# Performance work log

Hardware: AMD Instinct MI355X
Metric: run time of the kernel (lower is better)

Reference implementation:

```python
import jax, jax.numpy as jnp
import numpy as np

N_NODES = 100000
N_EDGES = 600000
N_GRAPHS = 64
EPS = 1e-5


def setup_inputs() -> dict:
    key = jax.random.key(0)
    ks = jax.random.split(key, 8)
    x = jax.random.normal(ks[0], (N_NODES, 128), dtype=jnp.float32)
    edge_index = jax.random.randint(ks[1], (2, N_EDGES), 0, N_NODES, dtype=jnp.int64)
    batch = jnp.sort(jax.random.randint(ks[2], (N_NODES,), 0, N_GRAPHS, dtype=jnp.int64))
    conv_w = jax.random.normal(ks[3], (6, 128, 128), dtype=jnp.float32) * (1.0 / np.sqrt(128))
    conv_b = jnp.zeros((6, 128), dtype=jnp.float32)
    bn_g = jnp.ones((6, 128), dtype=jnp.float32)
    bn_b = jnp.zeros((6, 128), dtype=jnp.float32)
    lin1_w = jax.random.normal(ks[4], (128, 64), dtype=jnp.float32) * (1.0 / np.sqrt(128))
    lin1_b = jnp.zeros((64,), dtype=jnp.float32)
    lin2_w = jax.random.normal(ks[5], (64, 4), dtype=jnp.float32) * (1.0 / np.sqrt(64))
    lin2_b = jnp.zeros((4,), dtype=jnp.float32)
    return {"x": x, "edge_index": edge_index, "batch": batch,
            "conv_w": conv_w, "conv_b": conv_b, "bn_g": bn_g, "bn_b": bn_b,
            "lin1_w": lin1_w, "lin1_b": lin1_b, "lin2_w": lin2_w, "lin2_b": lin2_b}


def reference(x, edge_index, batch, conv_w, conv_b, bn_g, bn_b, lin1_w, lin1_b, lin2_w, lin2_b):
    src, dst = edge_index[0], edge_index[1]  # messages flow src -> dst (PyG source_to_target)
    n = x.shape[0]
    h = x
    # 6 stacked GCNConv(normalize=False) -> ReLU -> BatchNorm1d (training-mode batch stats)
    for i in range(6):
        m = h @ conv_w[i]                                   # [N, H] transform first
        agg = jax.ops.segment_sum(m[src], dst, num_segments=n) + conv_b[i]
        h = jax.nn.relu(agg)
        mean = h.mean(axis=0)
        var = h.var(axis=0)                                  # biased, matches torch BN
        h = (h - mean) * jax.lax.rsqrt(var + EPS) * bn_g[i] + bn_b[i]
    # global mean pool over graphs
    s = jax.ops.segment_sum(h, batch, num_segments=N_GRAPHS)          # [G, H]
    cnt = jax.ops.segment_sum(jnp.ones((n,), h.dtype), batch, num_segments=N_GRAPHS)
    pooled = s / jnp.maximum(cnt, 1.0)[:, None]
    out = pooled @ lin1_w + lin1_b
    out = out @ lin2_w + lin2_b
    return jax.nn.log_softmax(out, axis=-1)
```

## Files before the change

kernel.cpp:

```cpp
#include <hip/hip_runtime.h>
#include <math.h>

#define NN 100000
#define NE 600000
#define NG 64
#define HD 128
#define NL 6
#define NB 1563
#define PSL 16

typedef unsigned short ushort_t;
typedef short short8 __attribute__((ext_vector_type(8)));
typedef float floatx4 __attribute__((ext_vector_type(4)));

__device__ __forceinline__ float bf2f(ushort_t u) {
    return __uint_as_float(((unsigned)u) << 16);
}
__device__ __forceinline__ ushort_t f2bf(float f) {
    unsigned u = __float_as_uint(f);
    unsigned r = (u + 0x7fffu + ((u >> 16) & 1u)) >> 16;
    return (ushort_t)r;
}


__global__ __launch_bounds__(256) void k_cast(const float* __restrict__ x,
                                              ushort_t* __restrict__ xb) {
    int i = blockIdx.x * 256 + threadIdx.x;
    if (i < NN * 32) {
        float4 v = ((const float4*)x)[i];
        ((ushort4*)xb)[i] = make_ushort4(f2bf(v.x), f2bf(v.y), f2bf(v.z), f2bf(v.w));
    }
}


__global__ __launch_bounds__(256) void k_wcast(const float* __restrict__ W,
                                               ushort_t* __restrict__ Wt) {
    const float* Wl = W + blockIdx.x * 16384;
    ushort_t* Wtl = Wt + blockIdx.x * 16384;
    for (int id = threadIdx.x; id < 16384; id += 256) {
        int k = id >> 7, c = id & 127;
        Wtl[c * 128 + k] = f2bf(Wl[id]);
    }
}


__global__ __launch_bounds__(256) void k_hist(const int* __restrict__ ei, int* __restrict__ counts) {
    int e = blockIdx.x * 256 + threadIdx.x;
    if (e < NE) atomicAdd(&counts[ei[NE + e]], 1);
}

__global__ __launch_bounds__(256) void k_scan1(const int* __restrict__ counts, int* __restrict__ bsums) {
    __shared__ int s[256];
    int i = blockIdx.x * 256 + threadIdx.x;
    s[threadIdx.x] = (i < NN) ? counts[i] : 0;
    __syncthreads();
    for (int off = 128; off > 0; off >>= 1) {
        if (threadIdx.x < off) s[threadIdx.x] += s[threadIdx.x + off];
        __syncthreads();
    }
    if (threadIdx.x == 0) bsums[blockIdx.x] = s[0];
}

__global__ __launch_bounds__(512) void k_scan2(int* __restrict__ bsums, int nb) {
    __shared__ int s[512];
    int t = threadIdx.x;
    s[t] = (t < nb) ? bsums[t] : 0;
    __syncthreads();
    for (int off = 1; off < 512; off <<= 1) {
        int v = (t >= off) ? s[t - off] : 0;
        __syncthreads();
        s[t] += v;
        __syncthreads();
    }
    if (t < nb) bsums[t] = (t == 0) ? 0 : s[t - 1];
}

__global__ __launch_bounds__(256) void k_scan3(const int* __restrict__ counts, const int* __restrict__ bsums,
                                               int* __restrict__ rowptr) {
    __shared__ int s[256];
    int t = threadIdx.x;
    int i = blockIdx.x * 256 + t;
    int v = (i < NN) ? counts[i] : 0;
    s[t] = v;
    __syncthreads();
    for (int off = 1; off < 256; off <<= 1) {
        int u = (t >= off) ? s[t - off] : 0;
        __syncthreads();
        s[t] += u;
        __syncthreads();
    }
    if (i < NN) rowptr[i] = bsums[blockIdx.x] + s[t] - v;
    if (i == 0) rowptr[NN] = NE;
}

__global__ __launch_bounds__(256) void k_fill(const int* __restrict__ ei, const int* __restrict__ rowptr,
                                              int* __restrict__ cursor, int* __restrict__ colsrc) {
    int e = blockIdx.x * 256 + threadIdx.x;
    if (e < NE) {
        int d = ei[NE + e];
        int pos = rowptr[d] + atomicAdd(&cursor[d], 1);
        colsrc[pos] = ei[e];
    }
}


__global__ __launch_bounds__(256) void k_dhist(const int* __restrict__ rowptr,
                                               int* __restrict__ dcount) {
    __shared__ int lc[64];
    int t = threadIdx.x;
    if (t < 64) lc[t] = 0;
    __syncthreads();
    int n = blockIdx.x * 256 + t;
    if (n < NN) {
        int d = rowptr[n + 1] - rowptr[n];
        atomicAdd(&lc[min(d, 63)], 1);
    }
    __syncthreads();
    if (t < 64 && lc[t] > 0) atomicAdd(&dcount[t], lc[t]);
}

__global__ __launch_bounds__(64) void k_dscan(const int* __restrict__ dcount,
                                              int* __restrict__ doff) {
    int t = threadIdx.x;
    int s = 0;
    for (int b = t + 1; b < 64; ++b) s += dcount[b];
    doff[t] = s;
}

__global__ __launch_bounds__(256) void k_dfill(const int* __restrict__ rowptr,
                                               const int* __restrict__ doff,
                                               int* __restrict__ dcursor,
                                               int* __restrict__ perm) {
    __shared__ int lc[64], lbase[64];
    int t = threadIdx.x;
    if (t < 64) lc[t] = 0;
    __syncthreads();
    int n = blockIdx.x * 256 + t;
    int b = 0, my = 0;
    if (n < NN) {
        int d = rowptr[n + 1] - rowptr[n];
        b = min(d, 63);
        my = atomicAdd(&lc[b], 1);
    }
    __syncthreads();
    if (t < 64 && lc[t] > 0) lbase[t] = atomicAdd(&dcursor[t], lc[t]);
    __syncthreads();
    if (n < NN) perm[doff[b] + lbase[b] + my] = n;
}


__global__ __launch_bounds__(256) void k_gconv(
    const ushort_t* __restrict__ hin, const int* __restrict__ perm,
    const int* __restrict__ rowptr, const int* __restrict__ colsrc,
    const float* __restrict__ stats, const float* __restrict__ bng,
    const float* __restrict__ bnb,
    const ushort_t* __restrict__ Wt, const float* __restrict__ bias,
    ushort_t* __restrict__ hout, float* __restrict__ partials) {
    __shared__ float sstat[256];
    int t = threadIdx.x;
    sstat[t] = 0.f;
    int wave = t >> 6, lane = t & 63;
    int l15 = lane & 15, quad = lane >> 4;
    int rowbase = blockIdx.x * 64 + wave * 16;
    int idx = rowbase + l15;
    bool valid = idx < NN;
    int row = valid ? perm[idx] : 0;
    int beg = valid ? rowptr[row] : 0;
    int end = valid ? rowptr[row + 1] : 0;
    int deg = end - beg;
    int maxd = deg;
    maxd = max(maxd, __shfl_xor(maxd, 1, 64));
    maxd = max(maxd, __shfl_xor(maxd, 2, 64));
    maxd = max(maxd, __shfl_xor(maxd, 4, 64));
    maxd = max(maxd, __shfl_xor(maxd, 8, 64));

    float ac[4][8];
    #pragma unroll
    for (int s = 0; s < 4; ++s)
        #pragma unroll
        for (int j = 0; j < 8; ++j) ac[s][j] = 0.f;

    const ushort_t* hbase = hin + quad * 8;
    int e = 0;
    for (; e + 1 < maxd; e += 2) {
        bool on0 = e < deg, on1 = e + 1 < deg;
        int i0 = on0 ? beg + e : 0;
        int i1 = on1 ? beg + e + 1 : 0;
        int s0 = colsrc[i0];
        int s1 = colsrc[i1];
        float m0 = on0 ? 1.f : 0.f;
        float m1 = on1 ? 1.f : 0.f;
        const short8* h0 = (const short8*)(hbase + (size_t)s0 * 128);
        const short8* h1 = (const short8*)(hbase + (size_t)s1 * 128);
        short8 v0[4], v1[4];
        #pragma unroll
        for (int s = 0; s < 4; ++s) { v0[s] = h0[s * 4]; v1[s] = h1[s * 4]; }
        #pragma unroll
        for (int s = 0; s < 4; ++s)
            #pragma unroll
            for (int j = 0; j < 8; ++j) {
                ac[s][j] = fmaf(m0, bf2f((ushort_t)v0[s][j]), ac[s][j]);
                ac[s][j] = fmaf(m1, bf2f((ushort_t)v1[s][j]), ac[s][j]);
            }
    }
    if (e < maxd) {
        bool on0 = e < deg;
        int i0 = on0 ? beg + e : 0;
        int s0 = colsrc[i0];
        float m0 = on0 ? 1.f : 0.f;
        const short8* h0 = (const short8*)(hbase + (size_t)s0 * 128);
        #pragma unroll
        for (int s = 0; s < 4; ++s) {
            short8 v0 = h0[s * 4];
            #pragma unroll
            for (int j = 0; j < 8; ++j)
                ac[s][j] = fmaf(m0, bf2f((ushort_t)v0[j]), ac[s][j]);
        }
    }

    float degf = (float)deg;
    short8 afrag[4];
    #pragma unroll
    for (int s = 0; s < 4; ++s) {
        short8 av;
        #pragma unroll
        for (int j = 0; j < 8; ++j) {
            int f = s * 32 + quad * 8 + j;
            float val;
            if (stats != nullptr) {
                const float inv_n = 1.0f / (float)NN;
                float m = stats[f] * inv_n;
                float var = fmaf(-m, m, stats[HD + f] * inv_n);
                float sc = bng[f] * rsqrtf(var + 1e-5f);
                float sh = bnb[f] - m * sc;
                val = fmaf(sc, ac[s][j], degf * sh);
            } else {
                val = ac[s][j];
            }
            av[j] = (short)f2bf(val);
        }
        afrag[s] = av;
    }

    floatx4 acc[8];
    #pragma unroll
    for (int c = 0; c < 8; ++c) acc[c] = (floatx4){0.f, 0.f, 0.f, 0.f};
    #pragma unroll
    for (int c = 0; c < 8; ++c) {
        size_t boff = (size_t)(16 * c + l15) * 128 + quad * 8;
        #pragma unroll
        for (int s = 0; s < 4; ++s) {
            short8 bf = *(const short8*)(Wt + boff + 32 * s);
            acc[c] = __builtin_amdgcn_mfma_f32_16x16x32_bf16(afrag[s], bf, acc[c], 0, 0, 0);
        }
    }

    int prow[4];
    #pragma unroll
    for (int i = 0; i < 4; ++i) prow[i] = __shfl(row, quad * 4 + i, 64);

    __syncthreads();
    int orow0 = rowbase + quad * 4;
    #pragma unroll
    for (int c = 0; c < 8; ++c) {
        int col = 16 * c + l15;
        float bv = bias[col];
        float ls = 0.f, lq = 0.f;
        #pragma unroll
        for (int i = 0; i < 4; ++i) {
            if (orow0 + i < NN) {
                float v = fmaxf(acc[c][i] + bv, 0.f);
                ushort_t bb = f2bf(v);
                hout[(size_t)prow[i] * 128 + col] = bb;
                float vr = bf2f(bb);
                ls += vr;
                lq = fmaf(vr, vr, lq);
            }
        }
        ls += __shfl_xor(ls, 16, 64);
        ls += __shfl_xor(ls, 32, 64);
        lq += __shfl_xor(lq, 16, 64);
        lq += __shfl_xor(lq, 32, 64);
        if (quad == 0) {
            atomicAdd(&sstat[col], ls);
            atomicAdd(&sstat[128 + col], lq);
        }
    }
    __syncthreads();
    partials[(size_t)blockIdx.x * 256 + t] = sstat[t];
}


__global__ __launch_bounds__(256) void k_red(const float* __restrict__ partials,
                                             float* __restrict__ stats) {
    int t = threadIdx.x;
    float s = 0.f;
    for (int r = blockIdx.x; r < NB; r += 64) s += partials[(size_t)r * 256 + t];
    atomicAdd(&stats[t], s);
}


__device__ __forceinline__ int lowerb(const int* __restrict__ b, int n, int key) {
    int lo = 0, hi = n;
    while (lo < hi) {
        int mid = (lo + hi) >> 1;
        if (b[mid] < key) lo = mid + 1;
        else hi = mid;
    }
    return lo;
}

__global__ __launch_bounds__(256) void k_pool1(
    const ushort_t* __restrict__ h, const int* __restrict__ batch,
    float* __restrict__ ppart) {
    int g = blockIdx.x >> 4;
    int sl = blockIdx.x & (PSL - 1);
    int lo = lowerb(batch, NN, g);
    int hi = lowerb(batch, NN, g + 1);
    int cnt = hi - lo;
    int a = lo + (int)(((long long)cnt * sl) >> 4);
    int b = lo + (int)(((long long)cnt * (sl + 1)) >> 4);
    int wave = threadIdx.x >> 6, lane = threadIdx.x & 63;
    const ushort2* h2 = (const ushort2*)h;
    float ax = 0.f, ay = 0.f;
    for (int n = a + wave; n < b; n += 4) {
        ushort2 v = h2[(size_t)n * 64 + lane];
        ax += bf2f(v.x);
        ay += bf2f(v.y);
    }
    __shared__ float2 red[4][64];
    red[wave][lane] = make_float2(ax, ay);
    __syncthreads();
    if (wave == 0) {
        float sx = 0.f, sy = 0.f;
        for (int w = 0; w < 4; ++w) {
            sx += red[w][lane].x;
            sy += red[w][lane].y;
        }
        ((float2*)ppart)[(size_t)blockIdx.x * 64 + lane] = make_float2(sx, sy);
    }
}


__global__ __launch_bounds__(64) void k_pool2(
    const float* __restrict__ ppart, const int* __restrict__ batch,
    const float* __restrict__ stats, const float* __restrict__ bng, const float* __restrict__ bnb,
    float* __restrict__ pooled) {
    int g = blockIdx.x;
    int lane = threadIdx.x;
    float sx = 0.f, sy = 0.f;
    #pragma unroll
    for (int s = 0; s < PSL; ++s) {
        float2 v = ((const float2*)ppart)[(size_t)(g * PSL + s) * 64 + lane];
        sx += v.x;
        sy += v.y;
    }
    int cnt = lowerb(batch, NN, g + 1) - lowerb(batch, NN, g);
    int c0 = lane * 2;
    const float inv_n = 1.0f / (float)NN;
    float m0 = stats[c0] * inv_n, m1 = stats[c0 + 1] * inv_n;
    float var0 = fmaf(-m0, m0, stats[HD + c0] * inv_n);
    float var1 = fmaf(-m1, m1, stats[HD + c0 + 1] * inv_n);
    float sc0 = bng[c0] * rsqrtf(var0 + 1e-5f);
    float sc1 = bng[c0 + 1] * rsqrtf(var1 + 1e-5f);
    float sh0 = bnb[c0] - m0 * sc0;
    float sh1 = bnb[c0 + 1] - m1 * sc1;
    float denom = fmaxf((float)cnt, 1.f);
    float2 o;
    o.x = (sc0 * sx + (float)cnt * sh0) / denom;
    o.y = (sc1 * sy + (float)cnt * sh1) / denom;
    ((float2*)pooled)[g * 64 + lane] = o;
}


__global__ __launch_bounds__(64) void k_head(
    const float* __restrict__ pooled, const float* __restrict__ w1, const float* __restrict__ b1,
    const float* __restrict__ w2, const float* __restrict__ b2, float* __restrict__ out) {
    int g = blockIdx.x;
    int j = threadIdx.x;
    float hid = b1[j];
    const float* p = pooled + g * 128;
    #pragma unroll 8
    for (int k = 0; k < 128; ++k) hid = fmaf(p[k], w1[k * 64 + j], hid);
    float o[4];
    #pragma unroll
    for (int c = 0; c < 4; ++c) {
        float v = hid * w2[j * 4 + c];
        #pragma unroll
        for (int off = 1; off < 64; off <<= 1) v += __shfl_xor(v, off, 64);
        o[c] = v + b2[c];
    }
    if (j == 0) {
        float mx = fmaxf(fmaxf(o[0], o[1]), fmaxf(o[2], o[3]));
        float se = expf(o[0] - mx) + expf(o[1] - mx) + expf(o[2] - mx) + expf(o[3] - mx);
        float ls = mx + logf(se);
        #pragma unroll
        for (int c = 0; c < 4; ++c) out[g * 4 + c] = o[c] - ls;
    }
}

extern "C" void kernel_launch(void* const* d_in, const int* in_sizes, int n_in,
                              void* d_out, int out_size, void* d_ws, size_t ws_size,
                              hipStream_t stream) {
    const float* x = (const float*)d_in[0];
    const int* ei = (const int*)d_in[1];
    const int* batch = (const int*)d_in[2];
    const float* conv_w = (const float*)d_in[3];
    const float* conv_b = (const float*)d_in[4];
    const float* bn_g = (const float*)d_in[5];
    const float* bn_b = (const float*)d_in[6];
    const float* l1w = (const float*)d_in[7];
    const float* l1b = (const float*)d_in[8];
    const float* l2w = (const float*)d_in[9];
    const float* l2b = (const float*)d_in[10];
    float* out = (float*)d_out;
    (void)in_sizes; (void)n_in; (void)out_size; (void)ws_size;

    char* ws = (char*)d_ws;
    int* counts = (int*)(ws + 0);
    int* dcount = (int*)(ws + 0);
    int* dcursor = (int*)(ws + 256);
    int* doff = (int*)(ws + 512);
    int* cursor = (int*)(ws + 400000);
    int* perm = (int*)(ws + 400000);
    float* stats = (float*)(ws + 800000);
    const size_t zero_bytes = 806144;
    int* rowptr = (int*)(ws + 806144);
    int* bsums = (int*)(ws + 1206400);
    int* colsrc = (int*)(ws + 1208192);
    float* pooled = (float*)(ws + 3608192);
    float* ppart = (float*)(ws + 3641344);
    float* partials = (float*)(ws + 4165632);
    ushort_t* xb = (ushort_t*)(ws + 5766656);
    ushort_t* hb0 = (ushort_t*)(ws + 31366656);
    ushort_t* hb1 = (ushort_t*)(ws + 56966656);
    ushort_t* wtbuf = (ushort_t*)(ws + 82566656);

    hipMemsetAsync(ws, 0, zero_bytes, stream);

    k_cast<<<(NN * 32 + 255) / 256, 256, 0, stream>>>(x, xb);
    k_wcast<<<NL, 256, 0, stream>>>(conv_w, wtbuf);

    int ebl = (NE + 255) / 256;
    int nb1 = (NN + 255) / 256;
    k_hist<<<ebl, 256, 0, stream>>>(ei, counts);
    k_scan1<<<nb1, 256, 0, stream>>>(counts, bsums);
    k_scan2<<<1, 512, 0, stream>>>(bsums, nb1);
    k_scan3<<<nb1, 256, 0, stream>>>(counts, bsums, rowptr);
    k_fill<<<ebl, 256, 0, stream>>>(ei, rowptr, cursor, colsrc);

    hipMemsetAsync(ws, 0, 512, stream);
    k_dhist<<<nb1, 256, 0, stream>>>(rowptr, dcount);
    k_dscan<<<1, 64, 0, stream>>>(dcount, doff);
    k_dfill<<<nb1, 256, 0, stream>>>(rowptr, doff, dcursor, perm);

    ushort_t* hb[2] = {hb0, hb1};
    for (int L = 0; L < NL; ++L) {
        const ushort_t* hin = (L == 0) ? xb : hb[(L + 1) & 1];
        ushort_t* hout = hb[L & 1];
        const float* lstats = (L == 0) ? nullptr : (stats + (L - 1) * 256);
        const float* lg = (L == 0) ? nullptr : (bn_g + (L - 1) * 128);
        const float* lb = (L == 0) ? nullptr : (bn_b + (L - 1) * 128);
        k_gconv<<<NB, 256, 0, stream>>>(hin, perm, rowptr, colsrc, lstats, lg, lb,
                                        wtbuf + L * 16384, conv_b + L * 128,
                                        hout, partials);
        k_red<<<64, 256, 0, stream>>>(partials, stats + L * 256);
    }
    k_pool1<<<NG * PSL, 256, 0, stream>>>(hb1, batch, ppart);
    k_pool2<<<NG, 64, 0, stream>>>(ppart, batch, stats + 5 * 256, bn_g + 5 * 128, bn_b + 5 * 128, pooled);
    k_head<<<NG, 64, 0, stream>>>(pooled, l1w, l1b, l2w, l2b, out);
}
```

Measured before the change: 762.8 us.

## Gather neighbor rows wave-cooperatively with coalesced loads staged through LDS

After: 765.9 us. Within noise of the previous version (+0.4%).

```diff
diff --git a/kernel.cpp b/kernel.cpp
--- a/kernel.cpp
+++ b/kernel.cpp
@@ -8,6 +8,7 @@
 #define NL 6
 #define NB 1563
 #define PSL 16
+#define ASTR 136
 
 typedef unsigned short ushort_t;
 typedef short short8 __attribute__((ext_vector_type(8)));
@@ -156,91 +157,97 @@
     const float* __restrict__ bnb,
     const ushort_t* __restrict__ Wt, const float* __restrict__ bias,
     ushort_t* __restrict__ hout, float* __restrict__ partials) {
+    __shared__ ushort_t Ab[64 * ASTR];
     __shared__ float sstat[256];
     int t = threadIdx.x;
     sstat[t] = 0.f;
     int wave = t >> 6, lane = t & 63;
     int l15 = lane & 15, quad = lane >> 4;
     int rowbase = blockIdx.x * 64 + wave * 16;
-    int idx = rowbase + l15;
-    bool valid = idx < NN;
-    int row = valid ? perm[idx] : 0;
-    int beg = valid ? rowptr[row] : 0;
-    int end = valid ? rowptr[row + 1] : 0;
-    int deg = end - beg;
-    int maxd = deg;
-    maxd = max(maxd, __shfl_xor(maxd, 1, 64));
-    maxd = max(maxd, __shfl_xor(maxd, 2, 64));
-    maxd = max(maxd, __shfl_xor(maxd, 4, 64));
-    maxd = max(maxd, __shfl_xor(maxd, 8, 64));
-
-    float ac[4][8];
+
+    float sc0 = 1.f, sc1 = 1.f, sh0 = 0.f, sh1 = 0.f;
+    {
+        int c0 = lane * 2;
+        if (stats != nullptr) {
+            const float inv_n = 1.0f / (float)NN;
+            float m0 = stats[c0] * inv_n, m1 = stats[c0 + 1] * inv_n;
+            float var0 = fmaf(-m0, m0, stats[HD + c0] * inv_n);
+            float var1 = fmaf(-m1, m1, stats[HD + c0 + 1] * inv_n);
+            sc0 = bng[c0] * rsqrtf(var0 + 1e-5f);
+            sc1 = bng[c0 + 1] * rsqrtf(var1 + 1e-5f);
+            sh0 = bnb[c0] - m0 * sc0;
+            sh1 = bnb[c0 + 1] - m1 * sc1;
+        }
+    }
+
+    const ushort2* h2 = (const ushort2*)hin;
+    #pragma unroll 1
+    for (int g = 0; g < 4; ++g) {
+        int b[4], d[4];
+        #pragma unroll
+        for (int i = 0; i < 4; ++i) {
+            int idx = rowbase + g * 4 + i;
+            bool v = idx < NN;
+            int r = v ? perm[idx] : 0;
+            b[i] = v ? rowptr[r] : 0;
+            int e2 = v ? rowptr[r + 1] : 0;
+            d[i] = e2 - b[i];
+        }
+        int maxd = max(max(d[0], d[1]), max(d[2], d[3]));
+        float ax[4] = {0.f, 0.f, 0.f, 0.f};
+        float ay[4] = {0.f, 0.f, 0.f, 0.f};
+        int e = 0;
+        for (; e + 1 < maxd; e += 2) {
+            int sa[4], sb[4];
+            float ma[4], mb[4];
+            #pragma unroll
+            for (int i = 0; i < 4; ++i) {
+                bool oa = e < d[i], ob = e + 1 < d[i];
+                sa[i] = colsrc[oa ? b[i] + e : 0];
+                sb[i] = colsrc[ob ? b[i] + e + 1 : 0];
+                ma[i] = oa ? 1.f : 0.f;
+                mb[i] = ob ? 1.f : 0.f;
+            }
+            ushort2 va[4], vb[4];
+            #pragma unroll
+            for (int i = 0; i < 4; ++i) {
+                va[i] = h2[(size_t)sa[i] * 64 + lane];
+                vb[i] = h2[(size_t)sb[i] * 64 + lane];
+            }
+            #pragma unroll
+            for (int i = 0; i < 4; ++i) {
+                ax[i] = fmaf(ma[i], bf2f(va[i].x), ax[i]);
+                ay[i] = fmaf(ma[i], bf2f(va[i].y), ay[i]);
+                ax[i] = fmaf(mb[i], bf2f(vb[i].x), ax[i]);
+                ay[i] = fmaf(mb[i], bf2f(vb[i].y), ay[i]);
+            }
+        }
+        if (e < maxd) {
+            #pragma unroll
+            for (int i = 0; i < 4; ++i) {
+                bool oa = e < d[i];
+                int s0 = colsrc[oa ? b[i] + e : 0];
+                float m0 = oa ? 1.f : 0.f;
+                ushort2 v0 = h2[(size_t)s0 * 64 + lane];
+                ax[i] = fmaf(m0, bf2f(v0.x), ax[i]);
+                ay[i] = fmaf(m0, bf2f(v0.y), ay[i]);
+            }
+        }
+        #pragma unroll
+        for (int i = 0; i < 4; ++i) {
+            float degf = (float)d[i];
+            float ox = fmaf(sc0, ax[i], degf * sh0);
+            float oy = fmaf(sc1, ay[i], degf * sh1);
+            int r = wave * 16 + g * 4 + i;
+            *(ushort2*)&Ab[r * ASTR + 2 * lane] = make_ushort2(f2bf(ox), f2bf(oy));
+        }
+    }
+    __syncthreads();
+
+    short8 afrag[4];
     #pragma unroll
     for (int s = 0; s < 4; ++s)
-        #pragma unroll
-        for (int j = 0; j < 8; ++j) ac[s][j] = 0.f;
-
-    const ushort_t* hbase = hin + quad * 8;
-    int e = 0;
-    for (; e + 1 < maxd; e += 2) {
-        bool on0 = e < deg, on1 = e + 1 < deg;
-        int i0 = on0 ? beg + e : 0;
-        int i1 = on1 ? beg + e + 1 : 0;
-        int s0 = colsrc[i0];
-        int s1 = colsrc[i1];
-        float m0 = on0 ? 1.f : 0.f;
-        float m1 = on1 ? 1.f : 0.f;
-        const short8* h0 = (const short8*)(hbase + (size_t)s0 * 128);
-        const short8* h1 = (const short8*)(hbase + (size_t)s1 * 128);
-        short8 v0[4], v1[4];
-        #pragma unroll
-        for (int s = 0; s < 4; ++s) { v0[s] = h0[s * 4]; v1[s] = h1[s * 4]; }
-        #pragma unroll
-        for (int s = 0; s < 4; ++s)
-            #pragma unroll
-            for (int j = 0; j < 8; ++j) {
-                ac[s][j] = fmaf(m0, bf2f((ushort_t)v0[s][j]), ac[s][j]);
-                ac[s][j] = fmaf(m1, bf2f((ushort_t)v1[s][j]), ac[s][j]);
-            }
-    }
-    if (e < maxd) {
-        bool on0 = e < deg;
-        int i0 = on0 ? beg + e : 0;
-        int s0 = colsrc[i0];
-        float m0 = on0 ? 1.f : 0.f;
-        const short8* h0 = (const short8*)(hbase + (size_t)s0 * 128);
-        #pragma unroll
-        for (int s = 0; s < 4; ++s) {
-            short8 v0 = h0[s * 4];
-            #pragma unroll
-            for (int j = 0; j < 8; ++j)
-                ac[s][j] = fmaf(m0, bf2f((ushort_t)v0[j]), ac[s][j]);
-        }
-    }
-
-    float degf = (float)deg;
-    short8 afrag[4];
-    #pragma unroll
-    for (int s = 0; s < 4; ++s) {
-        short8 av;
-        #pragma unroll
-        for (int j = 0; j < 8; ++j) {
-            int f = s * 32 + quad * 8 + j;
-            float val;
-            if (stats != nullptr) {
-                const float inv_n = 1.0f / (float)NN;
-                float m = stats[f] * inv_n;
-                float var = fmaf(-m, m, stats[HD + f] * inv_n);
-                float sc = bng[f] * rsqrtf(var + 1e-5f);
-                float sh = bnb[f] - m * sc;
-                val = fmaf(sc, ac[s][j], degf * sh);
-            } else {
-                val = ac[s][j];
-            }
-            av[j] = (short)f2bf(val);
-        }
-        afrag[s] = av;
-    }
+        afrag[s] = *(const short8*)&Ab[(wave * 16 + l15) * ASTR + quad * 8 + s * 32];
 
     floatx4 acc[8];
     #pragma unroll
@@ -257,9 +264,11 @@
 
     int prow[4];
     #pragma unroll
-    for (int i = 0; i < 4; ++i) prow[i] = __shfl(row, quad * 4 + i, 64);
-
-    __syncthreads();
+    for (int i = 0; i < 4; ++i) {
+        int idx = rowbase + quad * 4 + i;
+        prow[i] = (idx < NN) ? perm[idx] : 0;
+    }
+
     int orow0 = rowbase + quad * 4;
     #pragma unroll
     for (int c = 0; c < 8; ++c) {
```
